# Optimization experiments

Measured on AMD Instinct MI355X. Metric: run time of the kernel, lower is better.

The kernel has to match this reference:

```python
import jax, jax.numpy as jnp
import numpy as np

B, S, D, H = 2, 1024, 1024, 16
DK = D // H
NEG = -1000000000.0


def setup_inputs() -> dict:
    key = jax.random.key(0)
    ks = jax.random.split(key, 12)
    def lin(kw, kb):
        # torch nn.Linear default init: U(-1/sqrt(D), 1/sqrt(D))
        bound = 1.0 / np.sqrt(D)
        W = jax.random.uniform(kw, (D, D), jnp.float32, -bound, bound)
        b = jax.random.uniform(kb, (D,), jnp.float32, -bound, bound)
        return W, b
    Wq, bq = lin(ks[0], ks[1])
    Wk, bk = lin(ks[2], ks[3])
    Wv, bv = lin(ks[4], ks[5])
    Wo, bo = lin(ks[6], ks[7])
    q = jax.random.normal(ks[8], (B, S, D), jnp.float32)
    k = jax.random.normal(ks[9], (B, S, D), jnp.float32)
    v = jax.random.normal(ks[10], (B, S, D), jnp.float32)
    mask = jnp.ones((B, 1, S), jnp.int32)  # key-padding mask, 1 = keep
    return {"q": q, "k": k, "v": v, "mask": mask,
            "Wq": Wq, "bq": bq, "Wk": Wk, "bk": bk,
            "Wv": Wv, "bv": bv, "Wo": Wo, "bo": bo}


def reference(q, k, v, mask, Wq, bq, Wk, bk, Wv, bv, Wo, bo):
    b = q.shape[0]
    # projections -> [B, H, S, DK]
    def split_heads(x):
        return x.reshape(b, -1, H, DK).transpose(0, 2, 1, 3)
    qh = split_heads(q @ Wq.T + bq)
    kh = split_heads(k @ Wk.T + bk)
    vh = split_heads(v @ Wv.T + bv)
    # scores [B, H, S, S]
    scores = jnp.einsum('bhqd,bhkd->bhqk', qh, kh) / jnp.sqrt(jnp.float32(DK))
    m = mask[:, None]  # [B,1,1,S] broadcast over heads and query dim
    scores = jnp.where(m == 0, NEG, scores)
    attn = jax.nn.softmax(scores, axis=-1)  # dropout p=0.0 -> identity
    out = jnp.einsum('bhqk,bhkd->bhqd', attn, vh)
    concat = out.transpose(0, 2, 1, 3).reshape(b, -1, D)
    return concat @ Wo.T + bo
```

## Files before the change

### kernel.cpp

```cpp
#include <hip/hip_runtime.h>

#define H 16
#define DK 64
#define SD 1024
#define DD 1024
#define BB 2
#define MROWS (BB * SD)
#define KDIM 1024

typedef __attribute__((ext_vector_type(8))) short short8;
typedef __attribute__((ext_vector_type(4))) float floatx4;
typedef unsigned short u16;
typedef __attribute__((ext_vector_type(4))) unsigned short u16x4;

#if __has_builtin(__builtin_amdgcn_exp2f)
#define EXP2(x) __builtin_amdgcn_exp2f(x)
#else
#define EXP2(x) exp2f(x)
#endif
#if __has_builtin(__builtin_amdgcn_rcpf)
#define RCP(x) __builtin_amdgcn_rcpf(x)
#else
#define RCP(x) (1.0f / (x))
#endif

__device__ __forceinline__ u16 f2bf(float f) {
    union { float f; unsigned u; } v; v.f = f;
    unsigned u = v.u;
    return (u16)((u + 0x7FFFu + ((u >> 16) & 1u)) >> 16);
}

__device__ __forceinline__ void gload16(const void* g, void* l) {
    __builtin_amdgcn_global_load_lds((const __attribute__((address_space(1))) unsigned int*)g,
                                     (__attribute__((address_space(3))) unsigned int*)l, 16, 0, 0);
}

__global__ void cvt_all(const float4* __restrict__ q, const float4* __restrict__ k,
                        const float4* __restrict__ v, const float4* __restrict__ Wq,
                        const float4* __restrict__ Wk, const float4* __restrict__ Wv,
                        const float4* __restrict__ Wo, const int* __restrict__ mask,
                        u16x4* __restrict__ qb, u16x4* __restrict__ kb, u16x4* __restrict__ vb,
                        u16x4* __restrict__ Wqb, u16x4* __restrict__ Wkb, u16x4* __restrict__ Wvb,
                        u16x4* __restrict__ Wob, float* __restrict__ maskadd) {
    const int z = blockIdx.y;
    if (z == 7) {
        const int i = blockIdx.x * blockDim.x + threadIdx.x;
        if (i < BB * SD) maskadd[i] = (mask[i] != 0) ? 0.f : -1e9f;
        return;
    }
    const float4* src; u16x4* dst; int n4;
    switch (z) {
        case 0: src = q;  dst = qb;  n4 = MROWS * DD / 4; break;
        case 1: src = k;  dst = kb;  n4 = MROWS * DD / 4; break;
        case 2: src = v;  dst = vb;  n4 = MROWS * DD / 4; break;
        case 3: src = Wq; dst = Wqb; n4 = DD * DD / 4; break;
        case 4: src = Wk; dst = Wkb; n4 = DD * DD / 4; break;
        case 5: src = Wv; dst = Wvb; n4 = DD * DD / 4; break;
        default: src = Wo; dst = Wob; n4 = DD * DD / 4; break;
    }
    for (int i = blockIdx.x * blockDim.x + threadIdx.x; i < n4; i += gridDim.x * blockDim.x) {
        float4 f = src[i];
        u16x4 o;
        o.x = f2bf(f.x); o.y = f2bf(f.y); o.z = f2bf(f.z); o.w = f2bf(f.w);
        dst[i] = o;
    }
}

__device__ __forceinline__ void gemm_main64(const u16* __restrict__ A, const u16* __restrict__ W,
                                            u16* As, u16* Bs, floatx4 (&acc)[2][4],
                                            int row0, int col0) {
    const int tid = threadIdx.x;
    const int w = tid >> 6, lane = tid & 63, lg = lane >> 4, lr = lane & 15;
    const int lrow = lane >> 3;
    const int lcol = (lane & 7) * 8;

    const u16* Abase = A + (row0 + lrow) * KDIM + lcol;
    const u16* Wbase = W + (col0 + lrow) * KDIM + lcol;

#pragma unroll
    for (int j = 0; j < 4; j++) {
        const int seg = j * 4 + w;
        gload16(Abase + seg * 8 * KDIM, As + seg * 512);
    }
#pragma unroll
    for (int j = 0; j < 2; j++) {
        const int seg = j * 4 + w;
        gload16(Wbase + seg * 8 * KDIM, Bs + seg * 512);
    }
    __syncthreads();

    int buf = 0;
    for (int k0 = 0; k0 < KDIM; k0 += 64) {
        if (k0 + 64 < KDIM) {
            const int nb = buf ^ 1;
#pragma unroll
            for (int j = 0; j < 4; j++) {
                const int seg = j * 4 + w;
                gload16(Abase + seg * 8 * KDIM + k0 + 64, As + nb * 8192 + seg * 512);
            }
#pragma unroll
            for (int j = 0; j < 2; j++) {
                const int seg = j * 4 + w;
                gload16(Wbase + seg * 8 * KDIM + k0 + 64, Bs + nb * 4096 + seg * 512);
            }
        }
        const u16* Asb = As + buf * 8192;
        const u16* Bsb = Bs + buf * 4096;
        short8 af[2][2], bf[4][2];
#pragma unroll
        for (int kk = 0; kk < 2; kk++) {
#pragma unroll
            for (int mi = 0; mi < 2; mi++)
                af[mi][kk] = *(const short8*)&Asb[(w * 32 + mi * 16 + lr) * 64 + kk * 32 + lg * 8];
#pragma unroll
            for (int ni = 0; ni < 4; ni++)
                bf[ni][kk] = *(const short8*)&Bsb[(ni * 16 + lr) * 64 + kk * 32 + lg * 8];
        }
#pragma unroll
        for (int kk = 0; kk < 2; kk++)
#pragma unroll
            for (int mi = 0; mi < 2; mi++)
#pragma unroll
                for (int ni = 0; ni < 4; ni++)
                    acc[mi][ni] = __builtin_amdgcn_mfma_f32_16x16x32_bf16(af[mi][kk], bf[ni][kk], acc[mi][ni], 0, 0, 0);
        __syncthreads();
        buf ^= 1;
    }
}

__global__ __launch_bounds__(256) void gemm_qkv(const u16* __restrict__ qb, const u16* __restrict__ kb,
                                                const u16* __restrict__ vb, const u16* __restrict__ Wqb,
                                                const u16* __restrict__ Wkb, const u16* __restrict__ Wvb,
                                                const float* __restrict__ bq, const float* __restrict__ bk,
                                                const float* __restrict__ bv,
                                                u16* __restrict__ Qh, u16* __restrict__ Kf, u16* __restrict__ Vf) {
    __shared__ u16 As[2 * 128 * 64];
    __shared__ u16 Bs[2 * 64 * 64];
    const int id = blockIdx.x;
    const int xcd = id & 7, j = id >> 3;
    const int z = j >> 5, r = j & 31;
    const int by = (xcd << 1) | (r >> 4), bx = r & 15;

    const u16 *A, *W; const float* bias; u16* out; float scale;
    if (z == 0)      { A = qb; W = Wqb; bias = bq; out = Qh; scale = 0.18033688011112042f; }
    else if (z == 1) { A = kb; W = Wkb; bias = bk; out = Kf; scale = 1.f; }
    else             { A = vb; W = Wvb; bias = bv; out = Vf; scale = 1.f; }

    const int row0 = by * 128, col0 = bx * 64;
    floatx4 acc[2][4] = {};
    gemm_main64(A, W, As, Bs, acc, row0, col0);

    const int tid = threadIdx.x;
    const int w = tid >> 6, lane = tid & 63, lg = lane >> 4, lr = lane & 15;
#pragma unroll
    for (int mi = 0; mi < 2; mi++)
#pragma unroll
        for (int ni = 0; ni < 4; ni++) {
            const int col = col0 + ni * 16 + lr;
            const float bv_ = bias[col];
            const int h = col >> 6, dk = col & 63;
#pragma unroll
            for (int rr = 0; rr < 4; rr++) {
                const int row = row0 + w * 32 + mi * 16 + lg * 4 + rr;
                const int b = row >> 10, s = row & 1023;
                const int bh = b * H + h;
                const float val = (acc[mi][ni][rr] + bv_) * scale;
                if (z == 0) {
                    out[(bh * SD + s) * DK + dk] = f2bf(val);
                } else if (z == 1) {
                    out[bh * 65536 + (s >> 4) * 1024 + (dk >> 5) * 512 +
                        ((dk >> 3) & 3) * 128 + (s & 15) * 8 + (dk & 7)] = f2bf(val);
                } else {
                    out[bh * 65536 + (s >> 6) * 4096 + ((dk >> 4) * 2 + ((s >> 5) & 1)) * 512 +
                        ((s >> 3) & 3) * 128 + (dk & 15) * 8 + (s & 7)] = f2bf(val);
                }
            }
        }
}

__global__ __launch_bounds__(256) void gemm_o(const u16* __restrict__ A, const u16* __restrict__ W,
                                              const float* __restrict__ bias, float* __restrict__ out) {
    __shared__ u16 As[2 * 128 * 64];
    __shared__ u16 Bs[2 * 64 * 64];
    const int id = blockIdx.x;
    const int xcd = id & 7, j = id >> 3;
    const int by = (xcd << 1) | (j >> 4), bx = j & 15;
    const int row0 = by * 128, col0 = bx * 64;
    floatx4 acc[2][4] = {};
    gemm_main64(A, W, As, Bs, acc, row0, col0);

    const int tid = threadIdx.x;
    const int w = tid >> 6, lane = tid & 63, lg = lane >> 4, lr = lane & 15;
#pragma unroll
    for (int mi = 0; mi < 2; mi++)
#pragma unroll
        for (int ni = 0; ni < 4; ni++) {
            const int col = col0 + ni * 16 + lr;
            const float bv_ = bias[col];
#pragma unroll
            for (int rr = 0; rr < 4; rr++) {
                const int row = row0 + w * 32 + mi * 16 + lg * 4 + rr;
                out[row * DD + col] = acc[mi][ni][rr] + bv_;
            }
        }
}

__global__ __launch_bounds__(256, 4) void attn_fused(const u16* __restrict__ Qh,
                                                     const u16* __restrict__ Kf,
                                                     const u16* __restrict__ Vf,
                                                     const float* __restrict__ maskadd,
                                                     u16* __restrict__ attn) {
    __shared__ u16 KV[2][8192];
    __shared__ u16 Plds[4 * 16 * 64];
    const int id = blockIdx.x;
    const int xcd = id & 7, sblk = id >> 3;
    const int bh = (xcd << 2) | (sblk >> 4);
    const int qx = sblk & 15;
    const int b = bh >> 4, h = bh & 15;
    const int tid = threadIdx.x;
    const int w = tid >> 6, lane = tid & 63;
    const int lg = lane >> 4, lr = lane & 15;
    const int q0 = qx * 64 + w * 16;

    const u16* Qb = Qh + bh * SD * DK;
    const u16* Kb = Kf + bh * 65536;
    const u16* Vb = Vf + bh * 65536;
    const float* mb = maskadd + b * SD;

    short8 aq0 = *(const short8*)&Qb[(q0 + lr) * DK + lg * 8];
    short8 aq1 = *(const short8*)&Qb[(q0 + lr) * DK + 32 + lg * 8];

    floatx4 o[4] = {};
    float lsum[4] = {0.f, 0.f, 0.f, 0.f};

    const int NIT = SD / 64;
    const int c0 = w * 2, c1 = w * 2 + 1;

    const int prd0 = (w << 10) | (lr << 6) | ((lg ^ (lr & 7)) << 3);
    const int prd1 = (w << 10) | (lr << 6) | (((4 + lg) ^ (lr & 7)) << 3);

    gload16(Kb + c0 * 512 + lane * 8, &KV[0][c0 * 512]);
    gload16(Kb + c1 * 512 + lane * 8, &KV[0][c1 * 512]);
    gload16(Vb + c0 * 512 + lane * 8, &KV[0][4096 + c0 * 512]);
    gload16(Vb + c1 * 512 + lane * 8, &KV[0][4096 + c1 * 512]);
    __syncthreads();

    int buf = 0;
    for (int it = 0; it < NIT; ++it) {
        const int kv0 = it * 64;
        if (it + 1 < NIT) {
            const int nxt = (kv0 + 64) * 64;
            gload16(Kb + nxt + c0 * 512 + lane * 8, &KV[buf ^ 1][c0 * 512]);
            gload16(Kb + nxt + c1 * 512 + lane * 8, &KV[buf ^ 1][c1 * 512]);
            gload16(Vb + nxt + c0 * 512 + lane * 8, &KV[buf ^ 1][4096 + c0 * 512]);
            gload16(Vb + nxt + c1 * 512 + lane * 8, &KV[buf ^ 1][4096 + c1 * 512]);
        }
        const u16* Ks = &KV[buf][0];
        const u16* Vs = &KV[buf][4096];
#pragma unroll
        for (int ct = 0; ct < 4; ct++) {
            const float ma = mb[kv0 + ct * 16 + lr];
            short8 bk0 = *(const short8*)&Ks[ct * 1024 + lg * 128 + lr * 8];
            short8 bk1 = *(const short8*)&Ks[ct * 1024 + 512 + lg * 128 + lr * 8];
            floatx4 acc = {ma, ma, ma, ma};
            acc = __builtin_amdgcn_mfma_f32_16x16x32_bf16(aq0, bk0, acc, 0, 0, 0);
            acc = __builtin_amdgcn_mfma_f32_16x16x32_bf16(aq1, bk1, acc, 0, 0, 0);
#pragma unroll
            for (int rr = 0; rr < 4; rr++) {
                const float p = EXP2(acc[rr]);
                lsum[rr] += p;
                const int row = lg * 4 + rr;
                const int slot = (ct * 2 + (lr >> 3)) ^ (row & 7);
                Plds[(w << 10) | (row << 6) | (slot << 3) | (lr & 7)] = f2bf(p);
            }
        }
        short8 pa0 = *(const short8*)&Plds[prd0];
        short8 pa1 = *(const short8*)&Plds[prd1];
#pragma unroll
        for (int cd = 0; cd < 4; cd++) {
            short8 vb0 = *(const short8*)&Vs[cd * 1024 + lg * 128 + lr * 8];
            short8 vb1 = *(const short8*)&Vs[cd * 1024 + 512 + lg * 128 + lr * 8];
            o[cd] = __builtin_amdgcn_mfma_f32_16x16x32_bf16(pa0, vb0, o[cd], 0, 0, 0);
            o[cd] = __builtin_amdgcn_mfma_f32_16x16x32_bf16(pa1, vb1, o[cd], 0, 0, 0);
        }
        __syncthreads();
        buf ^= 1;
    }

#pragma unroll
    for (int rr = 0; rr < 4; rr++) {
        lsum[rr] += __shfl_xor(lsum[rr], 1);
        lsum[rr] += __shfl_xor(lsum[rr], 2);
        lsum[rr] += __shfl_xor(lsum[rr], 4);
        lsum[rr] += __shfl_xor(lsum[rr], 8);
    }

#pragma unroll
    for (int rr = 0; rr < 4; rr++) {
        const float inv = RCP(lsum[rr]);
        const int row = q0 + lg * 4 + rr;
#pragma unroll
        for (int cd = 0; cd < 4; cd++) {
            const int d = h * 64 + cd * 16 + lr;
            attn[(b * SD + row) * DD + d] = f2bf(o[cd][rr] * inv);
        }
    }
}

extern "C" void kernel_launch(void* const* d_in, const int* in_sizes, int n_in,
                              void* d_out, int out_size, void* d_ws, size_t ws_size,
                              hipStream_t stream) {
    const float* q  = (const float*)d_in[0];
    const float* k  = (const float*)d_in[1];
    const float* v  = (const float*)d_in[2];
    const int* mask = (const int*)d_in[3];
    const float* Wq = (const float*)d_in[4];
    const float* bq = (const float*)d_in[5];
    const float* Wk = (const float*)d_in[6];
    const float* bk = (const float*)d_in[7];
    const float* Wv = (const float*)d_in[8];
    const float* bv = (const float*)d_in[9];
    const float* Wo = (const float*)d_in[10];
    const float* bo = (const float*)d_in[11];
    float* out = (float*)d_out;

    u16* p = (u16*)d_ws;
    u16* qb  = p; p += MROWS * DD;
    u16* kb  = p; p += MROWS * DD;
    u16* vb  = p; p += MROWS * DD;
    u16* Wqb = p; p += DD * DD;
    u16* Wkb = p; p += DD * DD;
    u16* Wvb = p; p += DD * DD;
    u16* Wob = p; p += DD * DD;
    u16* Qh  = p; p += MROWS * DD;
    u16* Kf  = p; p += MROWS * DD;
    u16* Vf  = p; p += MROWS * DD;
    u16* attn = p; p += MROWS * DD;
    float* maskadd = (float*)p;

    cvt_all<<<dim3(512, 8), 256, 0, stream>>>((const float4*)q, (const float4*)k, (const float4*)v,
                                              (const float4*)Wq, (const float4*)Wk, (const float4*)Wv,
                                              (const float4*)Wo, mask,
                                              (u16x4*)qb, (u16x4*)kb, (u16x4*)vb,
                                              (u16x4*)Wqb, (u16x4*)Wkb, (u16x4*)Wvb, (u16x4*)Wob,
                                              maskadd);

    gemm_qkv<<<768, 256, 0, stream>>>(qb, kb, vb, Wqb, Wkb, Wvb, bq, bk, bv, Qh, Kf, Vf);

    attn_fused<<<512, 256, 0, stream>>>(Qh, Kf, Vf, maskadd, attn);

    gemm_o<<<256, 256, 0, stream>>>(attn, Wob, bo, out);
}
```

Baseline: 82.25 us.

## Use 64x64 tiles in output GEMM and raise MFMA wave priority in attention

The output projection GEMM now uses 64x64 tiles with its own inlined double-buffered main loop in place of the shared 128x64 helper, and launches 512 blocks instead of 256 so more CUs get work. Separately, the attention kernel wraps its MFMA sections in s_setprio so waves issuing matrix ops get scheduling priority over waves doing loads and exp. The smaller GEMM tiles give less reuse per block and load more operand traffic overall, and the priority hints may not help if the attention kernel is not bound by issue contention.

```diff
diff --git a/kernel.cpp b/kernel.cpp
--- a/kernel.cpp
+++ b/kernel.cpp
@@ -180,26 +180,74 @@
 
 __global__ __launch_bounds__(256) void gemm_o(const u16* __restrict__ A, const u16* __restrict__ W,
                                               const float* __restrict__ bias, float* __restrict__ out) {
-    __shared__ u16 As[2 * 128 * 64];
+    __shared__ u16 As[2 * 64 * 64];
     __shared__ u16 Bs[2 * 64 * 64];
     const int id = blockIdx.x;
     const int xcd = id & 7, j = id >> 3;
-    const int by = (xcd << 1) | (j >> 4), bx = j & 15;
-    const int row0 = by * 128, col0 = bx * 64;
-    floatx4 acc[2][4] = {};
-    gemm_main64(A, W, As, Bs, acc, row0, col0);
-
+    const int by = (xcd << 2) | (j >> 4), bx = j & 15;
+    const int row0 = by * 64, col0 = bx * 64;
     const int tid = threadIdx.x;
     const int w = tid >> 6, lane = tid & 63, lg = lane >> 4, lr = lane & 15;
+    const int wr = (w >> 1) * 32, wc = (w & 1) * 32;
+    const int lrow = lane >> 3;
+    const int lcol = (lane & 7) * 8;
+
+    const u16* Abase = A + (row0 + lrow) * KDIM + lcol;
+    const u16* Wbase = W + (col0 + lrow) * KDIM + lcol;
+
+    floatx4 acc[2][2] = {};
+
+#pragma unroll
+    for (int j2 = 0; j2 < 2; j2++) {
+        const int seg = j2 * 4 + w;
+        gload16(Abase + seg * 8 * KDIM, As + seg * 512);
+        gload16(Wbase + seg * 8 * KDIM, Bs + seg * 512);
+    }
+    __syncthreads();
+
+    int buf = 0;
+    for (int k0 = 0; k0 < KDIM; k0 += 64) {
+        if (k0 + 64 < KDIM) {
+            const int nb = buf ^ 1;
+#pragma unroll
+            for (int j2 = 0; j2 < 2; j2++) {
+                const int seg = j2 * 4 + w;
+                gload16(Abase + seg * 8 * KDIM + k0 + 64, As + nb * 4096 + seg * 512);
+                gload16(Wbase + seg * 8 * KDIM + k0 + 64, Bs + nb * 4096 + seg * 512);
+            }
+        }
+        const u16* Asb = As + buf * 4096;
+        const u16* Bsb = Bs + buf * 4096;
+        short8 af[2][2], bf[2][2];
+#pragma unroll
+        for (int kk = 0; kk < 2; kk++) {
+#pragma unroll
+            for (int mi = 0; mi < 2; mi++)
+                af[mi][kk] = *(const short8*)&Asb[(wr + mi * 16 + lr) * 64 + kk * 32 + lg * 8];
+#pragma unroll
+            for (int ni = 0; ni < 2; ni++)
+                bf[ni][kk] = *(const short8*)&Bsb[(wc + ni * 16 + lr) * 64 + kk * 32 + lg * 8];
+        }
+#pragma unroll
+        for (int kk = 0; kk < 2; kk++)
+#pragma unroll
+            for (int mi = 0; mi < 2; mi++)
+#pragma unroll
+                for (int ni = 0; ni < 2; ni++)
+                    acc[mi][ni] = __builtin_amdgcn_mfma_f32_16x16x32_bf16(af[mi][kk], bf[ni][kk], acc[mi][ni], 0, 0, 0);
+        __syncthreads();
+        buf ^= 1;
+    }
+
 #pragma unroll
     for (int mi = 0; mi < 2; mi++)
 #pragma unroll
-        for (int ni = 0; ni < 4; ni++) {
-            const int col = col0 + ni * 16 + lr;
+        for (int ni = 0; ni < 2; ni++) {
+            const int col = col0 + wc + ni * 16 + lr;
             const float bv_ = bias[col];
 #pragma unroll
             for (int rr = 0; rr < 4; rr++) {
-                const int row = row0 + w * 32 + mi * 16 + lg * 4 + rr;
+                const int row = row0 + wr + mi * 16 + lg * 4 + rr;
                 out[row * DD + col] = acc[mi][ni][rr] + bv_;
             }
         }
@@ -263,8 +311,10 @@
             short8 bk0 = *(const short8*)&Ks[ct * 1024 + lg * 128 + lr * 8];
             short8 bk1 = *(const short8*)&Ks[ct * 1024 + 512 + lg * 128 + lr * 8];
             floatx4 acc = {ma, ma, ma, ma};
+            __builtin_amdgcn_s_setprio(1);
             acc = __builtin_amdgcn_mfma_f32_16x16x32_bf16(aq0, bk0, acc, 0, 0, 0);
             acc = __builtin_amdgcn_mfma_f32_16x16x32_bf16(aq1, bk1, acc, 0, 0, 0);
+            __builtin_amdgcn_s_setprio(0);
 #pragma unroll
             for (int rr = 0; rr < 4; rr++) {
                 const float p = EXP2(acc[rr]);
@@ -276,6 +326,7 @@
         }
         short8 pa0 = *(const short8*)&Plds[prd0];
         short8 pa1 = *(const short8*)&Plds[prd1];
+        __builtin_amdgcn_s_setprio(1);
 #pragma unroll
         for (int cd = 0; cd < 4; cd++) {
             short8 vb0 = *(const short8*)&Vs[cd * 1024 + lg * 128 + lr * 8];
@@ -283,6 +334,7 @@
             o[cd] = __builtin_amdgcn_mfma_f32_16x16x32_bf16(pa0, vb0, o[cd], 0, 0, 0);
             o[cd] = __builtin_amdgcn_mfma_f32_16x16x32_bf16(pa1, vb1, o[cd], 0, 0, 0);
         }
+        __builtin_amdgcn_s_setprio(0);
         __syncthreads();
         buf ^= 1;
     }
@@ -349,5 +401,5 @@
 
     attn_fused<<<512, 256, 0, stream>>>(Qh, Kf, Vf, maskadd, attn);
 
-    gemm_o<<<256, 256, 0, stream>>>(attn, Wob, bo, out);
-}
+    gemm_o<<<512, 256, 0, stream>>>(attn, Wob, bo, out);
+}
```

Result: slower. 87.49 us (+6.4%).
